# Performance work log

Measured on AMD Instinct MI355X. Metric: run time of the kernel, lower is better.

The kernel has to match this reference:

```python
import jax, jax.numpy as jnp
import numpy as np

N_NODES = 20000
N_EDGES = 320000
HIDDEN = 512
EDGE_DIM = 64
LN_EPS = 1e-5


def mish(x):
    return x * jnp.tanh(jax.nn.softplus(x))


def setup_inputs() -> dict:
    key = jax.random.key(0)
    ks = jax.random.split(key, 8)
    s = lambda fan_in: 1.0 / np.sqrt(fan_in)
    return {
        "x": jax.random.normal(ks[0], (N_NODES, HIDDEN), dtype=jnp.float32),
        "edge_index": jax.random.randint(ks[1], (2, N_EDGES), 0, N_NODES, dtype=jnp.int64),
        "edge_attr": jax.random.normal(ks[2], (N_EDGES, EDGE_DIM), dtype=jnp.float32),
        "W1": jax.random.normal(ks[3], (2 * HIDDEN + EDGE_DIM, HIDDEN), dtype=jnp.float32) * s(2 * HIDDEN + EDGE_DIM),
        "b1": jnp.zeros((HIDDEN,), dtype=jnp.float32),
        "W2": jax.random.normal(ks[4], (HIDDEN, HIDDEN), dtype=jnp.float32) * s(HIDDEN),
        "b2": jnp.zeros((HIDDEN,), dtype=jnp.float32),
        "W3": jax.random.normal(ks[5], (2 * HIDDEN, HIDDEN), dtype=jnp.float32) * s(2 * HIDDEN),
        "b3": jnp.zeros((HIDDEN,), dtype=jnp.float32),
        "W4": jax.random.normal(ks[6], (HIDDEN, HIDDEN), dtype=jnp.float32) * s(HIDDEN),
        "b4": jnp.zeros((HIDDEN,), dtype=jnp.float32),
        "gamma": jnp.ones((HIDDEN,), dtype=jnp.float32),
        "beta": jnp.zeros((HIDDEN,), dtype=jnp.float32),
    }


def reference(x, edge_index, edge_attr, W1, b1, W2, b2, W3, b3, W4, b4, gamma, beta):
    src, dst = edge_index[0], edge_index[1]
    # msg_mlp: Linear -> Mish -> Linear -> Mish on [E, 2H+Edim]
    edge_feat = jnp.concatenate([x[src], x[dst], edge_attr], axis=-1)  # [E, 2H+Edim]
    h = mish(edge_feat @ W1 + b1)
    messages = mish(h @ W2 + b2)  # [E, H]
    # scatter-add messages to destination nodes
    agg = jax.ops.segment_sum(messages, dst, num_segments=x.shape[0])  # [N, H]
    # update_mlp: Linear -> Mish -> Linear
    u = mish(jnp.concatenate([x, agg], axis=-1) @ W3 + b3)
    out = u @ W4 + b4  # [N, H]
    # residual + LayerNorm
    y = x + out
    mu = jnp.mean(y, axis=-1, keepdims=True)
    var = jnp.mean(jnp.square(y - mu), axis=-1, keepdims=True)
    return (y - mu) * jax.lax.rsqrt(var + LN_EPS) * gamma + beta
```

## Files before the change

### kernel.cpp

```cpp
#include <hip/hip_runtime.h>
#include <cstdint>
#include <cstddef>

#define NNODES 20000
#define NEDGES 320000
#define HID 512
#define EDIM 64
#define KFEAT (2*HID + EDIM)

typedef __bf16 bf16x8 __attribute__((ext_vector_type(8)));
typedef short short8 __attribute__((ext_vector_type(8)));
typedef float f32x4 __attribute__((ext_vector_type(4)));

#define AM_NODE 1
#define AM_DIR  2
#define EP_BF16  0
#define EP_F32   2
#define EP_BF16L 3

__device__ __forceinline__ uint16_t f2bf(float f){
  uint32_t u = __float_as_uint(f);
  u += 0x7FFFu + ((u >> 16) & 1u);
  return (uint16_t)(u >> 16);
}
__device__ __forceinline__ float bf2f(uint16_t h){
  return __uint_as_float((uint32_t)h << 16);
}
__device__ __forceinline__ float mishf(float v){
  float e = __expf(fminf(v, 18.f));
  float n = e * (e + 2.f);
  return v * __fdividef(n, n + 2.f);
}
__device__ __forceinline__ void gl_lds16(const void* g, void* l){
  __builtin_amdgcn_global_load_lds(
      (const __attribute__((address_space(1))) uint32_t*)g,
      (__attribute__((address_space(3))) uint32_t*)l, 16, 0, 0);
}

__global__ void detect_idx(const int* __restrict__ e, int* __restrict__ flag){
  int i = blockIdx.x * 256 + threadIdx.x;
  if (e[2*i + 1] != 0) atomicOr(flag, 1);
}
__global__ void norm_idx(const int* __restrict__ e, const int* __restrict__ flag,
                         int* __restrict__ s, int* __restrict__ d){
  int i = blockIdx.x * 256 + threadIdx.x;
  if (i >= NEDGES) return;
  int sv, dv;
  if (*flag){ sv = e[i];     dv = e[NEDGES + i]; }
  else      { sv = e[2*i];   dv = e[2*NEDGES + 2*i]; }
  sv = sv < 0 ? 0 : (sv > NNODES-1 ? NNODES-1 : sv);
  dv = dv < 0 ? 0 : (dv > NNODES-1 ? NNODES-1 : dv);
  s[i] = sv; d[i] = dv;
}

__global__ void hist_k(const int* __restrict__ d, int* __restrict__ cnt){
  int i = blockIdx.x * 256 + threadIdx.x;
  if (i < NEDGES) atomicAdd(&cnt[d[i]], 1);
}
__global__ __launch_bounds__(256)
void scan_k(const int* __restrict__ cnt, int* __restrict__ rp, int* __restrict__ cur){
  const int SEG = (NNODES + 255) / 256;
  const int t = threadIdx.x;
  const int lo = t * SEG;
  const int hi = (lo + SEG < NNODES) ? lo + SEG : NNODES;
  int s = 0;
  for (int i = lo; i < hi; ++i) s += cnt[i];
  __shared__ int sh[256];
  sh[t] = s; __syncthreads();
  for (int o = 1; o < 256; o <<= 1){
    int v = (t >= o) ? sh[t - o] : 0;
    __syncthreads();
    sh[t] += v;
    __syncthreads();
  }
  int pre = t ? sh[t-1] : 0;
  for (int i = lo; i < hi; ++i){
    rp[i] = pre; cur[i] = pre; pre += cnt[i];
  }
  if (t == 255) rp[NNODES] = sh[255];
}
__global__ void permute_k(const int* __restrict__ srcN, const int* __restrict__ dstN,
                          int* __restrict__ cur, int* __restrict__ srcS,
                          int* __restrict__ eidx){
  int i = blockIdx.x * 256 + threadIdx.x;
  if (i < NEDGES){
    int d = dstN[i];
    int p = atomicAdd(&cur[d], 1);
    srcS[p] = srcN[i];
    eidx[p] = i;
  }
}
__global__ void fill_dstS(const int* __restrict__ rp, int* __restrict__ dstS){
  int n = blockIdx.x;
  int lo = rp[n], hi = rp[n+1];
  for (int e = lo + threadIdx.x; e < hi; e += 64) dstS[e] = n;
}

__global__ void cast_bf16_vec(const float4* __restrict__ in, ushort4* __restrict__ out, int n4){
  int i = blockIdx.x * 256 + threadIdx.x;
  if (i < n4){
    float4 v = in[i];
    ushort4 o; o.x = f2bf(v.x); o.y = f2bf(v.y); o.z = f2bf(v.z); o.w = f2bf(v.w);
    out[i] = o;
  }
}
__global__ void transpose_cast(const float* __restrict__ W, uint16_t* __restrict__ WT, int K, int N){
  int k = blockIdx.x * 256 + threadIdx.x;
  int n = blockIdx.y;
  if (k < K) WT[(size_t)n * K + k] = f2bf(W[(size_t)k * N + n]);
}

template<int AMODE, int EPI, int KTOT, int BPQ>
__global__ __launch_bounds__(256, 2)
void gemm_k(const uint16_t* __restrict__ A0, const uint16_t* __restrict__ A1,
            const uint16_t* __restrict__ BT, const float* __restrict__ bias,
            uint16_t* __restrict__ Cb, float* __restrict__ Cf,
            int bstr, int cstr, int m0base, int M, int crowOff)
{
  __shared__ __align__(16) char smem[32768];
  char* As = smem;
  char* Bs = smem + 16384;
  const int t = threadIdx.x;
  const int m0 = m0base + blockIdx.x * 128;
  const int n0 = blockIdx.y * 128;
  const int srow = t >> 3;
  const int c8   = t & 7;
  const int scol = ((c8 ^ (srow & 7)) << 3);
  const int ldst = srow * 128 + c8 * 16;

  const uint16_t* as0[4]; const uint16_t* as1[4];
  #pragma unroll
  for (int i = 0; i < 4; ++i){
    int gm = m0 + srow + 32*i;
    if (gm > M - 1) gm = M - 1;
    if (AMODE == AM_NODE){
      as0[i] = A0 + (size_t)gm * HID;
      as1[i] = A1 + (size_t)gm * HID;
    } else {
      as0[i] = A0 + (size_t)gm * KTOT;
      as1[i] = A0;
    }
  }
  const uint16_t* brow[4];
  #pragma unroll
  for (int i = 0; i < 4; ++i){
    int nr = n0 + srow + 32*i;
    if (BPQ) brow[i] = BT + (size_t)(nr & (HID-1))*bstr + (nr >> 9)*HID;
    else     brow[i] = BT + (size_t)nr*bstr;
  }

  const int lane = t & 63;
  const int wv = t >> 6;
  const int wm = (wv >> 1) * 64;
  const int wn = (wv & 1) * 64;
  const int l15 = lane & 15;
  const int lk16 = (lane >> 4) << 4;
  const int swz = (l15 & 7) << 4;

  f32x4 acc[4][4] = {};

  const int NK = KTOT / 64;
  for (int kk = 0; kk < NK; ++kk){
    const int k0 = kk * 64;
    #pragma unroll
    for (int i = 0; i < 4; ++i){
      const uint16_t* g;
      if (AMODE == AM_NODE){
        g = (k0 < HID) ? as0[i] + (k0 + scol) : as1[i] + (k0 - HID + scol);
      } else {
        g = as0[i] + (k0 + scol);
      }
      gl_lds16(g, As + i*4096 + ldst);
    }
    #pragma unroll
    for (int i = 0; i < 4; ++i)
      gl_lds16(brow[i] + (k0 + scol), Bs + i*4096 + ldst);
    __syncthreads();
    #pragma unroll
    for (int ks = 0; ks < 2; ++ks){
      bf16x8 af[4], bfr[4];
      #pragma unroll
      for (int i = 0; i < 4; ++i){
        const int ar = wm + i*16 + l15;
        af[i] = *(const bf16x8*)(As + ar*128 + ((ks*64 + lk16) ^ swz));
      }
      #pragma unroll
      for (int j = 0; j < 4; ++j){
        const int br = wn + j*16 + l15;
        bfr[j] = *(const bf16x8*)(Bs + br*128 + ((ks*64 + lk16) ^ swz));
      }
      #pragma unroll
      for (int i = 0; i < 4; ++i)
        #pragma unroll
        for (int j = 0; j < 4; ++j)
          acc[i][j] = __builtin_amdgcn_mfma_f32_16x16x32_bf16(af[i], bfr[j], acc[i][j], 0, 0, 0);
    }
    __syncthreads();
  }

  #pragma unroll
  for (int i = 0; i < 4; ++i){
    const int rb = wm + i*16 + ((lane >> 4) << 2);
    #pragma unroll
    for (int j = 0; j < 4; ++j){
      const int gcol = n0 + wn + j*16 + l15;
      const float bv = (EPI == EP_BF16L) ? 0.f : bias[gcol];
      #pragma unroll
      for (int r = 0; r < 4; ++r){
        const int grow = m0 + rb + r;
        if (grow < M){
          float v = acc[i][j][r] + bv;
          if (EPI == EP_BF16){
            Cb[(size_t)(grow - crowOff) * cstr + gcol] = f2bf(mishf(v));
          } else if (EPI == EP_BF16L){
            Cb[(size_t)(grow - crowOff) * cstr + gcol] = f2bf(v);
          } else {
            Cf[(size_t)grow * cstr + gcol] = v;
          }
        }
      }
    }
  }
}

__global__ __launch_bounds__(256, 4)
void eh_k(const uint16_t* __restrict__ eab, const uint16_t* __restrict__ PQb,
          const int* __restrict__ idx,
          const uint16_t* __restrict__ w1t, const float* __restrict__ b1,
          uint16_t* __restrict__ hb, int m0base, int crowOff)
{
  __shared__ __align__(16) char smem[32768];
  const int t = threadIdx.x;
  const int m0 = m0base + blockIdx.x * 32;
  const int lane = t & 63;
  const int wv = t >> 6;
  const int l15 = lane & 15;
  const int lg = lane >> 4;
  const int* srcS = idx;
  const int* dstS = idx + NEDGES;
  const int* eidx = idx + 2*NEDGES;

  int eidxr[2];
  #pragma unroll
  for (int fr = 0; fr < 2; ++fr) eidxr[fr] = eidx[m0 + fr*16 + l15];

  f32x4 acc[2][8] = {};

  #pragma unroll
  for (int ks = 0; ks < 2; ++ks){
    bf16x8 bF[8];
    #pragma unroll
    for (int fc = 0; fc < 8; ++fc){
      int n = wv*128 + fc*16 + l15;
      bF[fc] = *(const bf16x8*)(w1t + (size_t)n*KFEAT + 2*HID + ks*32 + lg*8);
    }
    #pragma unroll
    for (int fr = 0; fr < 2; ++fr){
      bf16x8 av = *(const bf16x8*)(eab + (size_t)eidxr[fr]*EDIM + ks*32 + lg*8);
      #pragma unroll
      for (int fc = 0; fc < 8; ++fc)
        acc[fr][fc] = __builtin_amdgcn_mfma_f32_16x16x32_bf16(av, bF[fc], acc[fr][fc], 0, 0, 0);
    }
  }

  char* slab = smem + wv*8192;
  const float4 b1v0 = *(const float4*)(b1 + wv*128 + l15*4);
  const float4 b1v1 = *(const float4*)(b1 + wv*128 + 64 + l15*4);
  #pragma unroll
  for (int fr = 0; fr < 2; ++fr){
    #pragma unroll
    for (int fc = 0; fc < 8; ++fc){
      #pragma unroll
      for (int r = 0; r < 4; ++r){
        int row = lg*4 + r;
        int cb = ((fc*16 + l15)*4) ^ ((lg & 1) << 6);
        *(float*)(slab + row*512 + cb) = acc[fr][fc][r];
      }
    }
    asm volatile("s_waitcnt lgkmcnt(0)" ::: "memory");
    __builtin_amdgcn_sched_barrier(0);
    #pragma unroll
    for (int i = 0; i < 4; ++i){
      int row = i*4 + lg;
      int grow = m0 + fr*16 + row;
      int s = srcS[grow];
      int d = dstS[grow];
      float4 v0 = *(const float4*)(slab + row*512 + ((l15*16) ^ ((i & 1) << 6)));
      float4 v1 = *(const float4*)(slab + row*512 + ((256 + l15*16) ^ ((i & 1) << 6)));
      ushort4 p0 = *(const ushort4*)(PQb + (size_t)s*1024 + wv*128 + l15*4);
      ushort4 p1 = *(const ushort4*)(PQb + (size_t)s*1024 + wv*128 + 64 + l15*4);
      ushort4 q0 = *(const ushort4*)(PQb + (size_t)d*1024 + 512 + wv*128 + l15*4);
      ushort4 q1 = *(const ushort4*)(PQb + (size_t)d*1024 + 512 + wv*128 + 64 + l15*4);
      ushort4 h0, h1;
      h0.x = f2bf(mishf(v0.x + bf2f(p0.x) + bf2f(q0.x) + b1v0.x));
      h0.y = f2bf(mishf(v0.y + bf2f(p0.y) + bf2f(q0.y) + b1v0.y));
      h0.z = f2bf(mishf(v0.z + bf2f(p0.z) + bf2f(q0.z) + b1v0.z));
      h0.w = f2bf(mishf(v0.w + bf2f(p0.w) + bf2f(q0.w) + b1v0.w));
      h1.x = f2bf(mishf(v1.x + bf2f(p1.x) + bf2f(q1.x) + b1v1.x));
      h1.y = f2bf(mishf(v1.y + bf2f(p1.y) + bf2f(q1.y) + b1v1.y));
      h1.z = f2bf(mishf(v1.z + bf2f(p1.z) + bf2f(q1.z) + b1v1.z));
      h1.w = f2bf(mishf(v1.w + bf2f(p1.w) + bf2f(q1.w) + b1v1.w));
      size_t hrow = (size_t)(grow - crowOff) * HID + wv*128;
      *(ushort4*)(hb + hrow + l15*4) = h0;
      *(ushort4*)(hb + hrow + 64 + l15*4) = h1;
    }
    asm volatile("s_waitcnt lgkmcnt(0)" ::: "memory");
    __builtin_amdgcn_sched_barrier(0);
  }
}

__global__ __launch_bounds__(128)
void gather_agg(const uint16_t* __restrict__ msg, const int* __restrict__ rp,
                float* __restrict__ agg, int e0, int e1){
  const int n = blockIdx.x;
  int lo = rp[n], hi = rp[n+1];
  if (lo < e0) lo = e0;
  if (hi > e1) hi = e1;
  if (lo >= hi) return;
  const int t = threadIdx.x;
  float4 a = {0.f, 0.f, 0.f, 0.f};
  for (int e = lo; e < hi; ++e){
    ushort4 m = ((const ushort4*)(msg + (size_t)(e - e0) * HID))[t];
    a.x += bf2f(m.x); a.y += bf2f(m.y); a.z += bf2f(m.z); a.w += bf2f(m.w);
  }
  float4* ap = ((float4*)(agg + (size_t)n * HID)) + t;
  float4 c = *ap;
  c.x += a.x; c.y += a.y; c.z += a.z; c.w += a.w;
  *ap = c;
}

__global__ __launch_bounds__(128)
void resid_ln(const float* __restrict__ x, const float* __restrict__ ob,
              const float* __restrict__ gamma, const float* __restrict__ beta,
              float* __restrict__ y){
  const int row = blockIdx.x;
  const int t = threadIdx.x;
  const float4 xv = ((const float4*)(x + (size_t)row * HID))[t];
  const float4 ov = ((const float4*)(ob + (size_t)row * HID))[t];
  float4 s4;
  s4.x = xv.x + ov.x; s4.y = xv.y + ov.y; s4.z = xv.z + ov.z; s4.w = xv.w + ov.w;
  float s = s4.x + s4.y + s4.z + s4.w;
  float q = s4.x*s4.x + s4.y*s4.y + s4.z*s4.z + s4.w*s4.w;
  #pragma unroll
  for (int o = 32; o; o >>= 1){
    s += __shfl_xor(s, o, 64);
    q += __shfl_xor(q, o, 64);
  }
  __shared__ float ss[2], qq[2];
  if ((t & 63) == 0){ ss[t >> 6] = s; qq[t >> 6] = q; }
  __syncthreads();
  const float S = ss[0] + ss[1], Q = qq[0] + qq[1];
  const float mu = S * (1.0f / HID);
  const float var = Q * (1.0f / HID) - mu * mu;
  const float inv = rsqrtf(var + 1e-5f);
  const float4 g = ((const float4*)gamma)[t];
  const float4 b = ((const float4*)beta)[t];
  float4 o;
  o.x = (s4.x - mu) * inv * g.x + b.x;
  o.y = (s4.y - mu) * inv * g.y + b.y;
  o.z = (s4.z - mu) * inv * g.z + b.z;
  o.w = (s4.w - mu) * inv * g.w + b.w;
  ((float4*)(y + (size_t)row * HID))[t] = o;
}

extern "C" void kernel_launch(void* const* d_in, const int* in_sizes, int n_in,
                              void* d_out, int out_size, void* d_ws, size_t ws_size,
                              hipStream_t stream)
{
  const float* x    = (const float*)d_in[0];
  const int*   ei   = (const int*)d_in[1];
  const float* ea   = (const float*)d_in[2];
  const float* W1   = (const float*)d_in[3];
  const float* b1   = (const float*)d_in[4];
  const float* W2   = (const float*)d_in[5];
  const float* b2   = (const float*)d_in[6];
  const float* W3   = (const float*)d_in[7];
  const float* b3   = (const float*)d_in[8];
  const float* W4   = (const float*)d_in[9];
  const float* b4   = (const float*)d_in[10];
  const float* gmm  = (const float*)d_in[11];
  const float* bet  = (const float*)d_in[12];
  float* out = (float*)d_out;

  uint8_t* w = (uint8_t*)d_ws;
  size_t off = 0;
  auto alloc = [&](size_t bytes) -> void* {
    void* p = w + off;
    off += (bytes + 255) & ~(size_t)255;
    return p;
  };
  uint16_t* xb   = (uint16_t*)alloc((size_t)NNODES*HID*2);
  uint16_t* w1t  = (uint16_t*)alloc((size_t)HID*KFEAT*2);
  uint16_t* w2t  = (uint16_t*)alloc((size_t)HID*HID*2);
  uint16_t* w3t  = (uint16_t*)alloc((size_t)HID*1024*2);
  uint16_t* w4t  = (uint16_t*)alloc((size_t)HID*HID*2);
  uint16_t* PQb  = (uint16_t*)alloc((size_t)NNODES*1024*2);
  float*    agg  = (float*)alloc((size_t)NNODES*HID*4);
  uint16_t* aggb = (uint16_t*)alloc((size_t)NNODES*HID*2);
  uint16_t* ub   = (uint16_t*)alloc((size_t)NNODES*HID*2);
  float*    outf = (float*)alloc((size_t)NNODES*HID*4);
  int*      srcN = (int*)alloc((size_t)NEDGES*4);
  int*      dstN = (int*)alloc((size_t)NEDGES*4);
  int*      idxS = (int*)alloc((size_t)NEDGES*4*3);
  int*      cnt  = (int*)alloc((size_t)NNODES*4);
  int*      rp   = (int*)alloc((size_t)(NNODES+1)*4);
  int*      cur  = (int*)alloc((size_t)NNODES*4);
  int*      flag = (int*)alloc(256);
  int*      srcS = idxS;
  int*      dstS = idxS + NEDGES;
  int*      eidx = idxS + 2*NEDGES;

  uint16_t* eab = (uint16_t*)outf;

  size_t remain = (ws_size > off) ? ws_size - off : 0;
  size_t maxChunk = remain / ((size_t)HID*2*2);
  long long chunkE = (long long)(maxChunk & ~(size_t)127);
  if (chunkE > NEDGES) chunkE = NEDGES;
  if (chunkE < 128) chunkE = 128;
  uint16_t* hb   = (uint16_t*)alloc((size_t)chunkE*HID*2);
  uint16_t* msgb = (uint16_t*)alloc((size_t)chunkE*HID*2);

  hipMemsetAsync(agg, 0, (size_t)NNODES*HID*4, stream);
  hipMemsetAsync(cnt, 0, (size_t)NNODES*4, stream);
  hipMemsetAsync(flag, 0, 4, stream);

  detect_idx<<<64, 256, 0, stream>>>(ei, flag);
  norm_idx<<<(NEDGES+255)/256, 256, 0, stream>>>(ei, flag, srcN, dstN);
  hist_k<<<(NEDGES+255)/256, 256, 0, stream>>>(dstN, cnt);
  scan_k<<<1, 256, 0, stream>>>(cnt, rp, cur);
  permute_k<<<(NEDGES+255)/256, 256, 0, stream>>>(srcN, dstN, cur, srcS, eidx);
  fill_dstS<<<NNODES, 64, 0, stream>>>(rp, dstS);

  cast_bf16_vec<<<(NNODES*HID/4+255)/256, 256, 0, stream>>>((const float4*)x, (ushort4*)xb, NNODES*HID/4);
  cast_bf16_vec<<<(NEDGES*EDIM/4+255)/256, 256, 0, stream>>>((const float4*)ea, (ushort4*)eab, NEDGES*EDIM/4);

  transpose_cast<<<dim3((KFEAT+255)/256, HID), 256, 0, stream>>>(W1, w1t, KFEAT, HID);
  transpose_cast<<<dim3((HID+255)/256,   HID), 256, 0, stream>>>(W2, w2t, HID, HID);
  transpose_cast<<<dim3((1024+255)/256,  HID), 256, 0, stream>>>(W3, w3t, 1024, HID);
  transpose_cast<<<dim3((HID+255)/256,   HID), 256, 0, stream>>>(W4, w4t, HID, HID);

  dim3 gpq((NNODES+127)/128, 1024/128);
  gemm_k<AM_DIR, EP_BF16L, HID, 1><<<gpq, 256, 0, stream>>>(
      xb, nullptr, w1t, b1, PQb, nullptr, KFEAT, 1024, 0, NNODES, 0);

  for (long long e0 = 0; e0 < NEDGES; e0 += chunkE){
    int ce = (int)((NEDGES - e0 < chunkE) ? (NEDGES - e0) : chunkE);
    eh_k<<<ce/32, 256, 0, stream>>>(eab, PQb, idxS, w1t, b1, hb, (int)e0, (int)e0);
    dim3 g2((ce+127)/128, HID/128);
    gemm_k<AM_DIR, EP_BF16, HID, 0><<<g2, 256, 0, stream>>>(
        hb, nullptr, w2t, b2, msgb, nullptr, HID, HID, 0, ce, 0);
    gather_agg<<<NNODES, 128, 0, stream>>>(msgb, rp, agg, (int)e0, (int)(e0+ce));
  }

  cast_bf16_vec<<<(NNODES*HID/4+255)/256, 256, 0, stream>>>((const float4*)agg, (ushort4*)aggb, NNODES*HID/4);

  dim3 g3((NNODES+127)/128, HID/128);
  gemm_k<AM_NODE, EP_BF16, 1024, 0><<<g3, 256, 0, stream>>>(
      xb, aggb, w3t, b3, ub, nullptr, 1024, HID, 0, NNODES, 0);
  gemm_k<AM_DIR, EP_F32, HID, 0><<<g3, 256, 0, stream>>>(
      ub, nullptr, w4t, b4, nullptr, outf, HID, HID, 0, NNODES, 0);

  resid_ln<<<NNODES, 128, 0, stream>>>(x, outf, gmm, bet, out);
}
```

Before: 967.2 us.

## Fuse scatter-add into message GEMM epilogue with segmented atomics

Replaces the separate bf16 message buffer and per-node gather kernel with an epilogue in the second message GEMM. The epilogue applies Mish and adds each sorted edge row into agg using atomics, merging runs of equal destination within a thread's four rows before each atomic. This removes the write and re-read of the message tensor and doubles the possible edge chunk size, since only one chunk buffer is needed. The grid is also transposed so column tiles vary fastest, which is meant to improve A-tile reuse in cache. The cost is many float atomics to agg and non-deterministic summation order.

Result: slower. 1.038 ms (+7.3%).

```diff
diff --git a/kernel.cpp b/kernel.cpp
--- a/kernel.cpp
+++ b/kernel.cpp
@@ -14,9 +14,10 @@
 
 #define AM_NODE 1
 #define AM_DIR  2
-#define EP_BF16  0
-#define EP_F32   2
-#define EP_BF16L 3
+#define EP_BF16    0
+#define EP_F32     2
+#define EP_BF16L   3
+#define EP_SCATSEG 4
 
 __device__ __forceinline__ uint16_t f2bf(float f){
   uint32_t u = __float_as_uint(f);
@@ -115,14 +116,15 @@
 void gemm_k(const uint16_t* __restrict__ A0, const uint16_t* __restrict__ A1,
             const uint16_t* __restrict__ BT, const float* __restrict__ bias,
             uint16_t* __restrict__ Cb, float* __restrict__ Cf,
+            const int* __restrict__ dstI,
             int bstr, int cstr, int m0base, int M, int crowOff)
 {
   __shared__ __align__(16) char smem[32768];
   char* As = smem;
   char* Bs = smem + 16384;
   const int t = threadIdx.x;
-  const int m0 = m0base + blockIdx.x * 128;
-  const int n0 = blockIdx.y * 128;
+  const int m0 = m0base + blockIdx.y * 128;
+  const int n0 = blockIdx.x * 128;
   const int srow = t >> 3;
   const int c8   = t & 7;
   const int scol = ((c8 ^ (srow & 7)) << 3);
@@ -201,21 +203,46 @@
   #pragma unroll
   for (int i = 0; i < 4; ++i){
     const int rb = wm + i*16 + ((lane >> 4) << 2);
+    int dstv[4];
+    if (EPI == EP_SCATSEG){
+      #pragma unroll
+      for (int r = 0; r < 4; ++r){
+        int grow = m0 + rb + r;
+        dstv[r] = (grow < M) ? dstI[grow] : -1;
+      }
+    }
     #pragma unroll
     for (int j = 0; j < 4; ++j){
       const int gcol = n0 + wn + j*16 + l15;
       const float bv = (EPI == EP_BF16L) ? 0.f : bias[gcol];
-      #pragma unroll
-      for (int r = 0; r < 4; ++r){
-        const int grow = m0 + rb + r;
-        if (grow < M){
-          float v = acc[i][j][r] + bv;
-          if (EPI == EP_BF16){
-            Cb[(size_t)(grow - crowOff) * cstr + gcol] = f2bf(mishf(v));
-          } else if (EPI == EP_BF16L){
-            Cb[(size_t)(grow - crowOff) * cstr + gcol] = f2bf(v);
-          } else {
-            Cf[(size_t)grow * cstr + gcol] = v;
+      if (EPI == EP_SCATSEG){
+        float part = 0.f; int cur = dstv[0];
+        #pragma unroll
+        for (int r = 0; r < 4; ++r){
+          int grow = m0 + rb + r;
+          if (grow < M){
+            float v = mishf(acc[i][j][r] + bv);
+            if (dstv[r] != cur){
+              if (cur >= 0) atomicAdd(&Cf[(size_t)cur * HID + gcol], part);
+              part = 0.f; cur = dstv[r];
+            }
+            part += v;
+          }
+        }
+        if (cur >= 0) atomicAdd(&Cf[(size_t)cur * HID + gcol], part);
+      } else {
+        #pragma unroll
+        for (int r = 0; r < 4; ++r){
+          const int grow = m0 + rb + r;
+          if (grow < M){
+            float v = acc[i][j][r] + bv;
+            if (EPI == EP_BF16){
+              Cb[(size_t)(grow - crowOff) * cstr + gcol] = f2bf(mishf(v));
+            } else if (EPI == EP_BF16L){
+              Cb[(size_t)(grow - crowOff) * cstr + gcol] = f2bf(v);
+            } else {
+              Cf[(size_t)grow * cstr + gcol] = v;
+            }
           }
         }
       }
@@ -307,26 +334,6 @@
     asm volatile("s_waitcnt lgkmcnt(0)" ::: "memory");
     __builtin_amdgcn_sched_barrier(0);
   }
-}
-
-__global__ __launch_bounds__(128)
-void gather_agg(const uint16_t* __restrict__ msg, const int* __restrict__ rp,
-                float* __restrict__ agg, int e0, int e1){
-  const int n = blockIdx.x;
-  int lo = rp[n], hi = rp[n+1];
-  if (lo < e0) lo = e0;
-  if (hi > e1) hi = e1;
-  if (lo >= hi) return;
-  const int t = threadIdx.x;
-  float4 a = {0.f, 0.f, 0.f, 0.f};
-  for (int e = lo; e < hi; ++e){
-    ushort4 m = ((const ushort4*)(msg + (size_t)(e - e0) * HID))[t];
-    a.x += bf2f(m.x); a.y += bf2f(m.y); a.z += bf2f(m.z); a.w += bf2f(m.w);
-  }
-  float4* ap = ((float4*)(agg + (size_t)n * HID)) + t;
-  float4 c = *ap;
-  c.x += a.x; c.y += a.y; c.z += a.z; c.w += a.w;
-  *ap = c;
 }
 
 __global__ __launch_bounds__(128)
@@ -413,12 +420,11 @@
   uint16_t* eab = (uint16_t*)outf;
 
   size_t remain = (ws_size > off) ? ws_size - off : 0;
-  size_t maxChunk = remain / ((size_t)HID*2*2);
+  size_t maxChunk = remain / ((size_t)HID*2);
   long long chunkE = (long long)(maxChunk & ~(size_t)127);
   if (chunkE > NEDGES) chunkE = NEDGES;
   if (chunkE < 128) chunkE = 128;
-  uint16_t* hb   = (uint16_t*)alloc((size_t)chunkE*HID*2);
-  uint16_t* msgb = (uint16_t*)alloc((size_t)chunkE*HID*2);
+  uint16_t* hb = (uint16_t*)alloc((size_t)chunkE*HID*2);
 
   hipMemsetAsync(agg, 0, (size_t)NNODES*HID*4, stream);
   hipMemsetAsync(cnt, 0, (size_t)NNODES*4, stream);
@@ -439,26 +445,25 @@
   transpose_cast<<<dim3((1024+255)/256,  HID), 256, 0, stream>>>(W3, w3t, 1024, HID);
   transpose_cast<<<dim3((HID+255)/256,   HID), 256, 0, stream>>>(W4, w4t, HID, HID);
 
-  dim3 gpq((NNODES+127)/128, 1024/128);
+  dim3 gpq(1024/128, (NNODES+127)/128);
   gemm_k<AM_DIR, EP_BF16L, HID, 1><<<gpq, 256, 0, stream>>>(
-      xb, nullptr, w1t, b1, PQb, nullptr, KFEAT, 1024, 0, NNODES, 0);
+      xb, nullptr, w1t, b1, PQb, nullptr, nullptr, KFEAT, 1024, 0, NNODES, 0);
 
   for (long long e0 = 0; e0 < NEDGES; e0 += chunkE){
     int ce = (int)((NEDGES - e0 < chunkE) ? (NEDGES - e0) : chunkE);
-    eh_k<<<ce/32, 256, 0, stream>>>(eab, PQb, idxS, w1t, b1, hb, (int)e0, (int)e0);
-    dim3 g2((ce+127)/128, HID/128);
-    gemm_k<AM_DIR, EP_BF16, HID, 0><<<g2, 256, 0, stream>>>(
-        hb, nullptr, w2t, b2, msgb, nullptr, HID, HID, 0, ce, 0);
-    gather_agg<<<NNODES, 128, 0, stream>>>(msgb, rp, agg, (int)e0, (int)(e0+ce));
+    eh_k<<<(ce+31)/32, 256, 0, stream>>>(eab, PQb, idxS, w1t, b1, hb, (int)e0, (int)e0);
+    dim3 g2(HID/128, (ce+127)/128);
+    gemm_k<AM_DIR, EP_SCATSEG, HID, 0><<<g2, 256, 0, stream>>>(
+        hb, nullptr, w2t, b2, nullptr, agg, dstS + e0, HID, HID, 0, ce, 0);
   }
 
   cast_bf16_vec<<<(NNODES*HID/4+255)/256, 256, 0, stream>>>((const float4*)agg, (ushort4*)aggb, NNODES*HID/4);
 
-  dim3 g3((NNODES+127)/128, HID/128);
+  dim3 g3(HID/128, (NNODES+127)/128);
   gemm_k<AM_NODE, EP_BF16, 1024, 0><<<g3, 256, 0, stream>>>(
-      xb, aggb, w3t, b3, ub, nullptr, 1024, HID, 0, NNODES, 0);
+      xb, aggb, w3t, b3, ub, nullptr, nullptr, 1024, HID, 0, NNODES, 0);
   gemm_k<AM_DIR, EP_F32, HID, 0><<<g3, 256, 0, stream>>>(
-      ub, nullptr, w4t, b4, nullptr, outf, HID, HID, 0, NNODES, 0);
+      ub, nullptr, w4t, b4, nullptr, outf, nullptr, HID, HID, 0, NNODES, 0);
 
   resid_ln<<<NNODES, 128, 0, stream>>>(x, outf, gmm, bet, out);
 }
```
